# Optimization experiments

Measured on AMD Instinct MI355X. Metric: run time of the kernel, lower is better.

The kernel has to match this reference:

```python
import jax, jax.numpy as jnp
import numpy as np

N, E, FIN, C, NCLS, L = 50000, 800000, 500, 128, 7, 8
ALPHA, THETA, NEG_SLOPE = 0.1, 0.5, 0.2


def _glorot(key, shape):
    # matches torch glorot: uniform(-sqrt(6/(fan_in+fan_out)))
    std = np.sqrt(6.0 / (shape[-2] + shape[-1])).astype(np.float32)
    return jax.random.uniform(key, shape, jnp.float32, -std, std)


def setup_inputs() -> dict:
    key = jax.random.key(0)
    ks = jax.random.split(key, 12)
    x = jax.random.normal(ks[0], (N, FIN), jnp.float32)
    edge_index = jax.random.randint(ks[1], (2, E), 0, N)
    return {
        "x": x,
        "edge_index": edge_index,
        "lin0_w": _glorot(ks[2], (FIN, C)),
        "lin0_b": jnp.zeros((C,), jnp.float32),
        "lin1_w": _glorot(ks[3], (C, NCLS)),
        "lin1_b": jnp.zeros((NCLS,), jnp.float32),
        "lin_w": _glorot(ks[4], (L, C, C)),   # shared lin_l == lin_r
        "att_l": _glorot(ks[5], (L, 1, C)).reshape(L, C),
        "att_r": _glorot(ks[6], (L, 1, C)).reshape(L, C),
        "w_p": _glorot(ks[7], (L, C, C)),
        "w_n": _glorot(ks[8], (L, C, C)),
        "w1": _glorot(ks[9], (L, C, C)),
    }


def reference(x, edge_index, lin0_w, lin0_b, lin1_w, lin1_b, lin_w, att_l, att_r, w_p, w_n, w1):
    # --- gcn_norm with self loops (identical every layer since cached topology) ---
    loop = jnp.arange(N)
    src = jnp.concatenate([edge_index[0], loop])  # [E'] sources (x_j)
    dst = jnp.concatenate([edge_index[1], loop])  # [E'] targets / scatter index (x_i)
    deg = jax.ops.segment_sum(jnp.ones(src.shape[0], jnp.float32), dst, num_segments=N)
    dinv = jnp.where(deg > 0, jax.lax.rsqrt(deg), 0.0)
    ew = dinv[src] * dinv[dst]  # symmetric norm, [E']

    x0 = jax.nn.relu(x @ lin0_w + lin0_b)  # [N, C]
    betas = jnp.log(THETA / jnp.arange(1, L + 1, dtype=jnp.float32) + 1.0)

    def layer(h, params):
        lw, al, ar, wp, wn, w1l, beta = params
        xl = h @ lw                              # lin_l(x), shared for l/r
        # per-edge gate: sigmoid(leaky_relu(sigma_j + sigma_i))
        s = jax.nn.sigmoid(jax.nn.leaky_relu((xl @ al)[src] + (xl @ ar)[dst], NEG_SLOPE))
        xp = h @ wp                              # source-side features
        xn = h @ wn                              # target-side features
        msg = ew[:, None] * (xp[src] * s[:, None] + xn[dst] * (1.0 - s[:, None]))  # [E', C]
        agg = jax.ops.segment_sum(msg, dst, num_segments=N)  # scatter-add
        hn = (1.0 - ALPHA) * agg + ALPHA * x0
        out = (1.0 - beta) * hn + beta * (hn @ w1l)  # addmm with weight2=None
        return jax.nn.relu(out), s

    h, sigmas = jax.lax.scan(layer, x0, (lin_w, att_l, att_r, w_p, w_n, w1, betas))
    logits = h @ lin1_w + lin1_b
    return jax.nn.log_softmax(logits, axis=-1), sigmas
```

## Files before the change

kernel.cpp:

```cpp
#include <hip/hip_runtime.h>
#include <math.h>

constexpr int NN   = 50000;
constexpr int NE   = 800000;
constexpr int EP   = NE + NN;
constexpr int FIN  = 500;
constexpr int KPAD = 512;
constexpr int C    = 128;
constexpr int NCLS = 7;
constexpr int NL   = 8;
constexpr float ALPHA = 0.1f;
constexpr float NEG_SLOPE = 0.2f;

typedef __bf16 bf16;
typedef __bf16 bf16x8 __attribute__((ext_vector_type(8)));
typedef float  f32x4  __attribute__((ext_vector_type(4)));

__device__ inline unsigned short f2bu(float f) {
    bf16 b = (bf16)f;
    return __builtin_bit_cast(unsigned short, b);
}
__device__ inline float bulo(unsigned u) { return __builtin_bit_cast(float, u << 16); }
__device__ inline float buhi(unsigned u) { return __builtin_bit_cast(float, u & 0xffff0000u); }

__global__ void fill_i32_k(int* p, int v, int n) {
    int i = blockIdx.x * blockDim.x + threadIdx.x;
    if (i < n) p[i] = v;
}

__global__ void count_deg_k(const int* __restrict__ dst, int* __restrict__ deg, int e) {
    int i = blockIdx.x * blockDim.x + threadIdx.x;
    if (i < e) atomicAdd(&deg[dst[i]], 1);
}

__global__ void dinv_k(const int* __restrict__ deg, float* __restrict__ dinv, int n) {
    int i = blockIdx.x * blockDim.x + threadIdx.x;
    if (i < n) dinv[i] = rsqrtf((float)deg[i]);
}

constexpr int SCB = 256;
constexpr int NSB = (NN + SCB - 1) / SCB;

__global__ __launch_bounds__(SCB) void scan1_k(const int* __restrict__ deg,
                                               int* __restrict__ exoff,
                                               int* __restrict__ bsum, int n) {
    __shared__ int s[SCB];
    int t = threadIdx.x;
    int i = blockIdx.x * SCB + t;
    int v = (i < n) ? deg[i] : 0;
    s[t] = v;
    __syncthreads();
    for (int off = 1; off < SCB; off <<= 1) {
        int u = (t >= off) ? s[t - off] : 0;
        __syncthreads();
        s[t] += u;
        __syncthreads();
    }
    if (i < n) exoff[i] = s[t] - v;
    if (t == SCB - 1) bsum[blockIdx.x] = s[t];
}

__global__ __launch_bounds__(SCB) void scan2_k(const int* __restrict__ bsum,
                                               int* __restrict__ boff, int nb) {
    __shared__ int s[SCB];
    int t = threadIdx.x;
    int v = (t < nb) ? bsum[t] : 0;
    s[t] = v;
    __syncthreads();
    for (int off = 1; off < SCB; off <<= 1) {
        int u = (t >= off) ? s[t - off] : 0;
        __syncthreads();
        s[t] += u;
        __syncthreads();
    }
    if (t < nb) boff[t] = s[t] - v;
}

__global__ __launch_bounds__(SCB) void scan3_k(const int* __restrict__ exoff,
                                               const int* __restrict__ boff,
                                               int* __restrict__ offs,
                                               int* __restrict__ cursor, int n) {
    int i = blockIdx.x * SCB + threadIdx.x;
    if (i < n) {
        int o = exoff[i] + boff[blockIdx.x];
        offs[i] = o;
        cursor[i] = o;
    }
    if (i == 0) offs[n] = EP;
}

__global__ void csr_fill_k(const int* __restrict__ src, const int* __restrict__ dst,
                           const float* __restrict__ dinv, int* __restrict__ cursor,
                           int2* __restrict__ csr2, int* __restrict__ pos_of) {
    int e = blockIdx.x * blockDim.x + threadIdx.x;
    if (e >= EP) return;
    int s, d;
    if (e < NE) { s = src[e]; d = dst[e]; }
    else { s = d = e - NE; }
    float ew = dinv[s] * dinv[d];
    int pos = atomicAdd(&cursor[d], 1);
    csr2[pos] = make_int2(s, __builtin_bit_cast(int, ew));
    pos_of[e] = pos;
}

__global__ void attproj_k(const float* __restrict__ lin_w, const float* __restrict__ att_l,
                          const float* __restrict__ att_r, float* __restrict__ alp,
                          float* __restrict__ arp) {
    __shared__ float al[C], ar[C];
    int l = blockIdx.x;
    int k = threadIdx.x;
    al[k] = att_l[l * C + k];
    ar[k] = att_r[l * C + k];
    __syncthreads();
    const float* w = lin_w + (size_t)l * C * C + (size_t)k * C;
    float s1 = 0.f, s2 = 0.f;
    #pragma unroll 8
    for (int c = 0; c < C; ++c) { float v = w[c]; s1 += v * al[c]; s2 += v * ar[c]; }
    alp[l * C + k] = s1;
    arp[l * C + k] = s2;
}

__global__ void wpn_trans_k(const float* __restrict__ w_p, const float* __restrict__ w_n,
                            bf16* __restrict__ out) {
    int l = blockIdx.y;
    int nt = blockIdx.x >> 2, kb = blockIdx.x & 3;
    int lane = threadIdx.x;
    const float* W = ((nt < 8) ? w_p : w_n) + (size_t)l * C * C;
    int col = (nt & 7) * 16 + (lane & 15);
    int k0 = kb * 32 + (lane >> 4) * 8;
    bf16* o = out + (((size_t)l * 16 * 4 + (size_t)(nt * 4 + kb)) * 64 + lane) * 8;
    #pragma unroll
    for (int j = 0; j < 8; ++j) o[j] = (bf16)W[(size_t)(k0 + j) * C + col];
}

__global__ void w1_trans_k(const float* __restrict__ w1, bf16* __restrict__ out) {
    int l = blockIdx.y;
    int nt = blockIdx.x >> 2, kb = blockIdx.x & 3;
    int lane = threadIdx.x;
    const float* W = w1 + (size_t)l * C * C;
    int col = nt * 16 + (lane & 15);
    int k0 = kb * 32 + (lane >> 4) * 8;
    bf16* o = out + (((size_t)l * 8 * 4 + (size_t)(nt * 4 + kb)) * 64 + lane) * 8;
    #pragma unroll
    for (int j = 0; j < 8; ++j) o[j] = (bf16)W[(size_t)(k0 + j) * C + col];
}

__global__ void lin0_trans_k(const float* __restrict__ w, bf16* __restrict__ out) {
    int nt = blockIdx.x >> 4, kb = blockIdx.x & 15;
    int lane = threadIdx.x;
    int col = nt * 16 + (lane & 15);
    int k0 = kb * 32 + (lane >> 4) * 8;
    bf16* o = out + (((size_t)(nt * 16 + kb)) * 64 + lane) * 8;
    #pragma unroll
    for (int j = 0; j < 8; ++j) {
        int k = k0 + j;
        o[j] = (bf16)((k < FIN) ? w[(size_t)k * C + col] : 0.f);
    }
}

__global__ __launch_bounds__(256) void conv_x_k(const float* __restrict__ x,
                                                unsigned* __restrict__ xb_u) {
    int gid = blockIdx.x * blockDim.x + threadIdx.x;
    if (gid >= NN * 64) return;
    int row = gid >> 6, cg = gid & 63;
    int col = cg * 8;
    float v[8];
    if (cg < 62) {
        const float4* p = (const float4*)(x + (size_t)row * FIN + col);
        float4 a = p[0], b = p[1];
        v[0] = a.x; v[1] = a.y; v[2] = a.z; v[3] = a.w;
        v[4] = b.x; v[5] = b.y; v[6] = b.z; v[7] = b.w;
    } else {
        #pragma unroll
        for (int j = 0; j < 8; ++j)
            v[j] = (col + j < FIN) ? x[(size_t)row * FIN + col + j] : 0.f;
    }
    uint4 o;
    o.x = (unsigned)f2bu(v[0]) | ((unsigned)f2bu(v[1]) << 16);
    o.y = (unsigned)f2bu(v[2]) | ((unsigned)f2bu(v[3]) << 16);
    o.z = (unsigned)f2bu(v[4]) | ((unsigned)f2bu(v[5]) << 16);
    o.w = (unsigned)f2bu(v[6]) | ((unsigned)f2bu(v[7]) << 16);
    *(uint4*)(xb_u + (size_t)row * 256 + cg * 4) = o;
}

template <int NT, int KB, int MODE>
__global__ __launch_bounds__(256) void mgemm_k(const bf16* __restrict__ Ab,
                                               const bf16* __restrict__ Wt, int M,
                                               const float* __restrict__ bias, float beta,
                                               float* __restrict__ out_f,
                                               bf16* __restrict__ out_b,
                                               const float* __restrict__ alp,
                                               const float* __restrict__ arp,
                                               float* __restrict__ sl,
                                               float* __restrict__ sr,
                                               float* __restrict__ sig_out,
                                               const float* __restrict__ sigc,
                                               const int* __restrict__ pos_of) {
    if (MODE == 2) {
        int gid = blockIdx.x * 256 + threadIdx.x;
        int stride = gridDim.x * 256;
        for (int e = gid; e < EP; e += stride) sig_out[e] = sigc[pos_of[e]];
    }
    const int lane = threadIdx.x & 63;
    const int wv = threadIdx.x >> 6;
    const int m0 = blockIdx.x * 64 + wv * 16;
    const int mrow = lane & 15;
    const int quad = lane >> 4;
    int arow = m0 + mrow;
    if (arow >= M) arow = M - 1;
    const bf16* Arow = Ab + (size_t)arow * (KB * 32) + quad * 8;
    const bf16x8* wbase = reinterpret_cast<const bf16x8*>(Wt) + (size_t)lane;

    f32x4 acc[NT];
    #pragma unroll
    for (int t = 0; t < NT; ++t) acc[t] = (f32x4){0.f, 0.f, 0.f, 0.f};

    #pragma unroll
    for (int kb = 0; kb < KB; ++kb) {
        bf16x8 a = *reinterpret_cast<const bf16x8*>(Arow + kb * 32);
        #pragma unroll
        for (int t = 0; t < NT; ++t) {
            bf16x8 b = wbase[(size_t)(t * KB + kb) * 64];
            acc[t] = __builtin_amdgcn_mfma_f32_16x16x32_bf16(a, b, acc[t], 0, 0, 0);
        }
    }

    constexpr int NC = NT * 16;
    #pragma unroll
    for (int t = 0; t < NT; ++t) {
        int col = t * 16 + mrow;
        #pragma unroll
        for (int r = 0; r < 4; ++r) {
            int row = m0 + quad * 4 + r;
            float v = acc[t][r];
            if (MODE == 1) v = fmaxf(v + bias[col], 0.f);
            if (MODE == 2) {
                float h = (row < M) ? (float)Ab[(size_t)row * NC + col] : 0.f;
                v = fmaxf((1.f - beta) * h + beta * v, 0.f);
            }
            acc[t][r] = v;
            if (row < M) {
                if (MODE == 2 && out_f != nullptr) out_f[(size_t)row * NC + col] = v;
                out_b[(size_t)row * NC + col] = (bf16)v;
            }
        }
    }
    if ((MODE == 1 || MODE == 2) && sl != nullptr) {
        float sa[4] = {0.f, 0.f, 0.f, 0.f}, sb[4] = {0.f, 0.f, 0.f, 0.f};
        #pragma unroll
        for (int t = 0; t < NT; ++t) {
            float av = alp[t * 16 + mrow];
            float bv = arp[t * 16 + mrow];
            #pragma unroll
            for (int r = 0; r < 4; ++r) {
                sa[r] += acc[t][r] * av;
                sb[r] += acc[t][r] * bv;
            }
        }
        #pragma unroll
        for (int r = 0; r < 4; ++r) {
            #pragma unroll
            for (int m = 1; m < 16; m <<= 1) {
                sa[r] += __shfl_xor(sa[r], m);
                sb[r] += __shfl_xor(sb[r], m);
            }
        }
        if (mrow == 0) {
            #pragma unroll
            for (int r = 0; r < 4; ++r) {
                int row = m0 + quad * 4 + r;
                if (row < M) { sl[row] = sa[r]; sr[row] = sb[r]; }
            }
        }
    }
}

__global__ __launch_bounds__(256) void agg_k(const int* __restrict__ offs,
                                             const int2* __restrict__ csr2,
                                             const float* __restrict__ sl,
                                             const float* __restrict__ sr,
                                             const unsigned* __restrict__ xpnb_u,
                                             const unsigned* __restrict__ x0b_u,
                                             float* __restrict__ sigc,
                                             unsigned* __restrict__ hnb_u, int n) {
    int wid = (blockIdx.x * blockDim.x + threadIdx.x) >> 6;
    int lane = threadIdx.x & 63;
    if (wid >= n) return;
    int s0 = offs[wid], s1 = offs[wid + 1];
    float srw = sr[wid];
    const int g = lane >> 4;
    const int cg = lane & 15;
    float acc[8];
    #pragma unroll
    for (int i = 0; i < 8; ++i) acc[i] = 0.f;
    float cnl = 0.f;

    for (int j0 = s0; j0 < s1; j0 += 64) {
        int j = j0 + lane;
        int msrc = 0;
        float mcoef = 0.f;
        if (j < s1) {
            int2 e = csr2[j];
            float ew = __builtin_bit_cast(float, e.y);
            float xg = sl[e.x] + srw;
            float lr = (xg > 0.f) ? xg : NEG_SLOPE * xg;
            float sg = 1.f / (1.f + expf(-lr));
            sigc[j] = sg;
            msrc = e.x;
            mcoef = ew * sg;
            cnl += ew * (1.f - sg);
        }
        int cnt = min(64, s1 - j0);
        for (int t = 0; t < cnt; t += 4) {
            int idx = t + g;
            float coef = __shfl(mcoef, idx);
            int srcn = __shfl(msrc, idx);
            uint4 v = *(const uint4*)(xpnb_u + (size_t)srcn * 128 + cg * 4);
            acc[0] += coef * bulo(v.x);
            acc[1] += coef * buhi(v.x);
            acc[2] += coef * bulo(v.y);
            acc[3] += coef * buhi(v.y);
            acc[4] += coef * bulo(v.z);
            acc[5] += coef * buhi(v.z);
            acc[6] += coef * bulo(v.w);
            acc[7] += coef * buhi(v.w);
        }
    }
    #pragma unroll
    for (int i = 0; i < 8; ++i) {
        acc[i] += __shfl_xor(acc[i], 16);
        acc[i] += __shfl_xor(acc[i], 32);
    }
    #pragma unroll
    for (int m = 1; m < 64; m <<= 1) cnl += __shfl_xor(cnl, m);
    unsigned un = xpnb_u[(size_t)wid * 128 + 64 + cg * 4 + g];
    unsigned u0 = x0b_u[(size_t)wid * 64 + cg * 4 + g];
    float ox = (1.f - ALPHA) * (acc[g * 2] + cnl * bulo(un)) + ALPHA * bulo(u0);
    float oy = (1.f - ALPHA) * (acc[g * 2 + 1] + cnl * buhi(un)) + ALPHA * buhi(u0);
    hnb_u[(size_t)wid * 64 + cg * 4 + g] = (unsigned)f2bu(ox) | ((unsigned)f2bu(oy) << 16);
}

__global__ __launch_bounds__(256) void logits_k(const float* __restrict__ h,
                                                const float* __restrict__ w,
                                                const float* __restrict__ b,
                                                float* __restrict__ out, int n) {
    __shared__ float ws[C * NCLS];
    __shared__ float bs[NCLS];
    for (int i = threadIdx.x; i < C * NCLS; i += 256) ws[i] = w[i];
    if (threadIdx.x < NCLS) bs[threadIdx.x] = b[threadIdx.x];
    __syncthreads();
    int i = blockIdx.x * blockDim.x + threadIdx.x;
    if (i >= n) return;
    const float4* hr = (const float4*)(h + (size_t)i * C);
    float acc[NCLS];
    #pragma unroll
    for (int c = 0; c < NCLS; ++c) acc[c] = 0.f;
    for (int k4 = 0; k4 < C / 4; ++k4) {
        float4 v = hr[k4];
        int k = k4 * 4;
        #pragma unroll
        for (int c = 0; c < NCLS; ++c) {
            acc[c] += v.x * ws[k * NCLS + c] + v.y * ws[(k + 1) * NCLS + c] +
                      v.z * ws[(k + 2) * NCLS + c] + v.w * ws[(k + 3) * NCLS + c];
        }
    }
    float lg[NCLS], m = -1e30f;
    #pragma unroll
    for (int c = 0; c < NCLS; ++c) { lg[c] = acc[c] + bs[c]; m = fmaxf(m, lg[c]); }
    float sum = 0.f;
    #pragma unroll
    for (int c = 0; c < NCLS; ++c) sum += expf(lg[c] - m);
    float lse = m + logf(sum);
    #pragma unroll
    for (int c = 0; c < NCLS; ++c) out[(size_t)i * NCLS + c] = lg[c] - lse;
}

extern "C" void kernel_launch(void* const* d_in, const int* in_sizes, int n_in,
                              void* d_out, int out_size, void* d_ws, size_t ws_size,
                              hipStream_t stream) {
    (void)in_sizes; (void)n_in; (void)out_size; (void)ws_size;
    const float* x      = (const float*)d_in[0];
    const int*   eidx   = (const int*)d_in[1];
    const float* lin0_w = (const float*)d_in[2];
    const float* lin0_b = (const float*)d_in[3];
    const float* lin1_w = (const float*)d_in[4];
    const float* lin1_b = (const float*)d_in[5];
    const float* lin_w  = (const float*)d_in[6];
    const float* att_l  = (const float*)d_in[7];
    const float* att_r  = (const float*)d_in[8];
    const float* w_p    = (const float*)d_in[9];
    const float* w_n    = (const float*)d_in[10];
    const float* w1     = (const float*)d_in[11];
    float* outp = (float*)d_out;
    float* sig_base = outp + (size_t)NN * NCLS;

    const int* srcA = eidx;
    const int* dstA = eidx + NE;

    float* f = (float*)d_ws;
    float* hF   = f; f += (size_t)NN * C;
    float* sl   = f; f += NN;
    float* sr   = f; f += NN;
    float* sigc = f; f += EP;
    float* dinv = f; f += NN;
    float* alp  = f; f += NL * C;
    float* arp  = f; f += NL * C;
    f += (4 - ((NN * 2 + EP + NN + 2 * NL * C) & 3)) & 3;
    bf16* bp = (bf16*)f;
    bf16* xb    = bp;
    bf16* xpnb  = bp;  bp += (size_t)NN * 2 * C;
    bf16* hnb   = bp;  bp += (size_t)NN * C;
    bf16* hb    = bp;  bp += (size_t)NN * C;
    bf16* x0b   = bp;  bp += (size_t)NN * C;
    bf16* wpnt  = bp;  bp += (size_t)NL * 16 * 4 * 64 * 8;
    bf16* w1t   = bp;  bp += (size_t)NL * 8 * 4 * 64 * 8;
    bf16* lin0t = bp;  bp += (size_t)8 * 16 * 64 * 8;
    int* ip = (int*)bp;
    int* deg     = ip; ip += NN;
    int* offs    = ip; ip += NN + 4;
    int* cursor  = ip; ip += NN;
    int* pos_of  = ip; ip += EP;
    int* exoff   = ip; ip += NN;
    int* bsum    = ip; ip += SCB;
    int* boff    = ip; ip += SCB;
    ip += (ip - (int*)d_ws) & 1;
    int2* csr2   = (int2*)ip; ip += 2 * EP;

    dim3 B(256);
    int gN   = (NN + 255) / 256;
    int gE   = (NE + 255) / 256;
    int gEP  = (EP + 255) / 256;
    int gM64 = (NN + 63) / 64;
    int gAgg = NN / 4;

    fill_i32_k<<<gN, B, 0, stream>>>(deg, 1, NN);
    count_deg_k<<<gE, B, 0, stream>>>(dstA, deg, NE);
    dinv_k<<<gN, B, 0, stream>>>(deg, dinv, NN);
    scan1_k<<<NSB, SCB, 0, stream>>>(deg, exoff, bsum, NN);
    scan2_k<<<1, SCB, 0, stream>>>(bsum, boff, NSB);
    scan3_k<<<NSB, SCB, 0, stream>>>(exoff, boff, offs, cursor, NN);
    csr_fill_k<<<gEP, B, 0, stream>>>(srcA, dstA, dinv, cursor, csr2, pos_of);
    attproj_k<<<NL, C, 0, stream>>>(lin_w, att_l, att_r, alp, arp);

    wpn_trans_k<<<dim3(64, NL), 64, 0, stream>>>(w_p, w_n, wpnt);
    w1_trans_k<<<dim3(32, NL), 64, 0, stream>>>(w1, w1t);
    lin0_trans_k<<<128, 64, 0, stream>>>(lin0_w, lin0t);
    conv_x_k<<<(NN * 64 + 255) / 256, B, 0, stream>>>(x, (unsigned*)xb);

    mgemm_k<8, 16, 1><<<gM64, B, 0, stream>>>(xb, lin0t, NN, lin0_b, 0.f,
                                              nullptr, x0b, alp, arp, sl, sr,
                                              nullptr, nullptr, nullptr);

    const bf16* curb = x0b;
    for (int l = 0; l < NL; ++l) {
        float beta = (float)log(0.5 / (double)(l + 1) + 1.0);
        bool last = (l == NL - 1);
        mgemm_k<16, 4, 0><<<gM64, B, 0, stream>>>(curb, wpnt + (size_t)l * 16 * 4 * 64 * 8,
                                                  NN, nullptr, 0.f, nullptr, xpnb,
                                                  nullptr, nullptr, nullptr, nullptr,
                                                  nullptr, nullptr, nullptr);
        agg_k<<<gAgg, B, 0, stream>>>(offs, csr2, sl, sr, (const unsigned*)xpnb,
                                      (const unsigned*)x0b, sigc, (unsigned*)hnb, NN);
        mgemm_k<8, 4, 2><<<gM64, B, 0, stream>>>(hnb, w1t + (size_t)l * 8 * 4 * 64 * 8,
                                                 NN, nullptr, beta,
                                                 last ? hF : nullptr, hb,
                                                 last ? nullptr : (alp + (l + 1) * C),
                                                 last ? nullptr : (arp + (l + 1) * C),
                                                 last ? nullptr : sl,
                                                 last ? nullptr : sr,
                                                 sig_base + (size_t)l * EP, sigc, pos_of);
        curb = hb;
    }

    logits_k<<<gN, B, 0, stream>>>(hF, lin1_w, lin1_b, outp, NN);
}
```

Measured before the change: 981.0 us.

## Recompute per-edge sigmoid in original order instead of caching via pos_of scatter

Removes the sigc cache and pos_of permutation. Sigmas are now recomputed directly in original edge order inside the MODE 0 GEMM prologue from sl/sr and the raw edge index, so agg_k no longer writes per-edge sigmoid values. Setup kernels are also consolidated: the degree fill and dinv kernels are folded into a memset and scan1, and the three weight-transpose kernels become one pack kernel. A zero-coefficient skip is added in the gather loop. The trade-off is duplicated sigmoid math and random sl/sr reads in exchange for less memory traffic and fewer launches.

Result: slower. 1.218 ms (+24.1%).

```diff
diff --git a/kernel.cpp b/kernel.cpp
--- a/kernel.cpp
+++ b/kernel.cpp
@@ -5,7 +5,6 @@
 constexpr int NE   = 800000;
 constexpr int EP   = NE + NN;
 constexpr int FIN  = 500;
-constexpr int KPAD = 512;
 constexpr int C    = 128;
 constexpr int NCLS = 7;
 constexpr int NL   = 8;
@@ -23,31 +22,23 @@
 __device__ inline float bulo(unsigned u) { return __builtin_bit_cast(float, u << 16); }
 __device__ inline float buhi(unsigned u) { return __builtin_bit_cast(float, u & 0xffff0000u); }
 
-__global__ void fill_i32_k(int* p, int v, int n) {
-    int i = blockIdx.x * blockDim.x + threadIdx.x;
-    if (i < n) p[i] = v;
-}
-
 __global__ void count_deg_k(const int* __restrict__ dst, int* __restrict__ deg, int e) {
     int i = blockIdx.x * blockDim.x + threadIdx.x;
     if (i < e) atomicAdd(&deg[dst[i]], 1);
 }
 
-__global__ void dinv_k(const int* __restrict__ deg, float* __restrict__ dinv, int n) {
-    int i = blockIdx.x * blockDim.x + threadIdx.x;
-    if (i < n) dinv[i] = rsqrtf((float)deg[i]);
-}
-
 constexpr int SCB = 256;
 constexpr int NSB = (NN + SCB - 1) / SCB;
 
 __global__ __launch_bounds__(SCB) void scan1_k(const int* __restrict__ deg,
                                                int* __restrict__ exoff,
-                                               int* __restrict__ bsum, int n) {
+                                               int* __restrict__ bsum,
+                                               float* __restrict__ dinv, int n) {
     __shared__ int s[SCB];
     int t = threadIdx.x;
     int i = blockIdx.x * SCB + t;
-    int v = (i < n) ? deg[i] : 0;
+    int v = (i < n) ? deg[i] + 1 : 0;
+    if (i < n) dinv[i] = rsqrtf((float)v);
     s[t] = v;
     __syncthreads();
     for (int off = 1; off < SCB; off <<= 1) {
@@ -91,7 +82,7 @@
 
 __global__ void csr_fill_k(const int* __restrict__ src, const int* __restrict__ dst,
                            const float* __restrict__ dinv, int* __restrict__ cursor,
-                           int2* __restrict__ csr2, int* __restrict__ pos_of) {
+                           int2* __restrict__ csr2) {
     int e = blockIdx.x * blockDim.x + threadIdx.x;
     if (e >= EP) return;
     int s, d;
@@ -100,7 +91,6 @@
     float ew = dinv[s] * dinv[d];
     int pos = atomicAdd(&cursor[d], 1);
     csr2[pos] = make_int2(s, __builtin_bit_cast(int, ew));
-    pos_of[e] = pos;
 }
 
 __global__ void attproj_k(const float* __restrict__ lin_w, const float* __restrict__ att_l,
@@ -120,41 +110,42 @@
     arp[l * C + k] = s2;
 }
 
-__global__ void wpn_trans_k(const float* __restrict__ w_p, const float* __restrict__ w_n,
-                            bf16* __restrict__ out) {
-    int l = blockIdx.y;
-    int nt = blockIdx.x >> 2, kb = blockIdx.x & 3;
+__global__ void pack_k(const float* __restrict__ w_p, const float* __restrict__ w_n,
+                       const float* __restrict__ w1, const float* __restrict__ lin0_w,
+                       bf16* __restrict__ wpnt, bf16* __restrict__ w1t,
+                       bf16* __restrict__ lin0t) {
+    int b = blockIdx.x;
     int lane = threadIdx.x;
-    const float* W = ((nt < 8) ? w_p : w_n) + (size_t)l * C * C;
-    int col = (nt & 7) * 16 + (lane & 15);
-    int k0 = kb * 32 + (lane >> 4) * 8;
-    bf16* o = out + (((size_t)l * 16 * 4 + (size_t)(nt * 4 + kb)) * 64 + lane) * 8;
-    #pragma unroll
-    for (int j = 0; j < 8; ++j) o[j] = (bf16)W[(size_t)(k0 + j) * C + col];
-}
-
-__global__ void w1_trans_k(const float* __restrict__ w1, bf16* __restrict__ out) {
-    int l = blockIdx.y;
-    int nt = blockIdx.x >> 2, kb = blockIdx.x & 3;
-    int lane = threadIdx.x;
-    const float* W = w1 + (size_t)l * C * C;
-    int col = nt * 16 + (lane & 15);
-    int k0 = kb * 32 + (lane >> 4) * 8;
-    bf16* o = out + (((size_t)l * 8 * 4 + (size_t)(nt * 4 + kb)) * 64 + lane) * 8;
-    #pragma unroll
-    for (int j = 0; j < 8; ++j) o[j] = (bf16)W[(size_t)(k0 + j) * C + col];
-}
-
-__global__ void lin0_trans_k(const float* __restrict__ w, bf16* __restrict__ out) {
-    int nt = blockIdx.x >> 4, kb = blockIdx.x & 15;
-    int lane = threadIdx.x;
-    int col = nt * 16 + (lane & 15);
-    int k0 = kb * 32 + (lane >> 4) * 8;
-    bf16* o = out + (((size_t)(nt * 16 + kb)) * 64 + lane) * 8;
-    #pragma unroll
-    for (int j = 0; j < 8; ++j) {
-        int k = k0 + j;
-        o[j] = (bf16)((k < FIN) ? w[(size_t)k * C + col] : 0.f);
+    if (b < NL * 64) {
+        int l = b >> 6, inner = b & 63;
+        int nt = inner >> 2, kb = inner & 3;
+        const float* W = ((nt < 8) ? w_p : w_n) + (size_t)l * C * C;
+        int col = (nt & 7) * 16 + (lane & 15);
+        int k0 = kb * 32 + (lane >> 4) * 8;
+        bf16* o = wpnt + (((size_t)l * 64 + inner) * 64 + lane) * 8;
+        #pragma unroll
+        for (int j = 0; j < 8; ++j) o[j] = (bf16)W[(size_t)(k0 + j) * C + col];
+    } else if (b < NL * 96) {
+        int idx = b - NL * 64;
+        int l = idx >> 5, inner = idx & 31;
+        int nt = inner >> 2, kb = inner & 3;
+        const float* W = w1 + (size_t)l * C * C;
+        int col = nt * 16 + (lane & 15);
+        int k0 = kb * 32 + (lane >> 4) * 8;
+        bf16* o = w1t + (((size_t)l * 32 + inner) * 64 + lane) * 8;
+        #pragma unroll
+        for (int j = 0; j < 8; ++j) o[j] = (bf16)W[(size_t)(k0 + j) * C + col];
+    } else {
+        int idx = b - NL * 96;
+        int nt = idx >> 4, kb = idx & 15;
+        int col = nt * 16 + (lane & 15);
+        int k0 = kb * 32 + (lane >> 4) * 8;
+        bf16* o = lin0t + (((size_t)(nt * 16 + kb)) * 64 + lane) * 8;
+        #pragma unroll
+        for (int j = 0; j < 8; ++j) {
+            int k = k0 + j;
+            o[j] = (bf16)((k < FIN) ? lin0_w[(size_t)k * C + col] : 0.f);
+        }
     }
 }
 
@@ -194,12 +185,19 @@
                                                float* __restrict__ sl,
                                                float* __restrict__ sr,
                                                float* __restrict__ sig_out,
-                                               const float* __restrict__ sigc,
-                                               const int* __restrict__ pos_of) {
-    if (MODE == 2) {
+                                               const int* __restrict__ srcA,
+                                               const int* __restrict__ dstA) {
+    if (MODE == 0) {
         int gid = blockIdx.x * 256 + threadIdx.x;
         int stride = gridDim.x * 256;
-        for (int e = gid; e < EP; e += stride) sig_out[e] = sigc[pos_of[e]];
+        for (int e = gid; e < EP; e += stride) {
+            int s, d;
+            if (e < NE) { s = srcA[e]; d = dstA[e]; }
+            else { s = d = e - NE; }
+            float xg = sl[s] + sr[d];
+            float lr = (xg > 0.f) ? xg : NEG_SLOPE * xg;
+            sig_out[e] = 1.f / (1.f + expf(-lr));
+        }
     }
     const int lane = threadIdx.x & 63;
     const int wv = threadIdx.x >> 6;
@@ -245,7 +243,7 @@
             }
         }
     }
-    if ((MODE == 1 || MODE == 2) && sl != nullptr) {
+    if ((MODE == 1 || MODE == 2) && alp != nullptr) {
         float sa[4] = {0.f, 0.f, 0.f, 0.f}, sb[4] = {0.f, 0.f, 0.f, 0.f};
         #pragma unroll
         for (int t = 0; t < NT; ++t) {
@@ -281,7 +279,6 @@
                                              const float* __restrict__ sr,
                                              const unsigned* __restrict__ xpnb_u,
                                              const unsigned* __restrict__ x0b_u,
-                                             float* __restrict__ sigc,
                                              unsigned* __restrict__ hnb_u, int n) {
     int wid = (blockIdx.x * blockDim.x + threadIdx.x) >> 6;
     int lane = threadIdx.x & 63;
@@ -305,7 +302,6 @@
             float xg = sl[e.x] + srw;
             float lr = (xg > 0.f) ? xg : NEG_SLOPE * xg;
             float sg = 1.f / (1.f + expf(-lr));
-            sigc[j] = sg;
             msrc = e.x;
             mcoef = ew * sg;
             cnl += ew * (1.f - sg);
@@ -315,15 +311,17 @@
             int idx = t + g;
             float coef = __shfl(mcoef, idx);
             int srcn = __shfl(msrc, idx);
-            uint4 v = *(const uint4*)(xpnb_u + (size_t)srcn * 128 + cg * 4);
-            acc[0] += coef * bulo(v.x);
-            acc[1] += coef * buhi(v.x);
-            acc[2] += coef * bulo(v.y);
-            acc[3] += coef * buhi(v.y);
-            acc[4] += coef * bulo(v.z);
-            acc[5] += coef * buhi(v.z);
-            acc[6] += coef * bulo(v.w);
-            acc[7] += coef * buhi(v.w);
+            if (coef != 0.f) {
+                uint4 v = *(const uint4*)(xpnb_u + (size_t)srcn * 128 + cg * 4);
+                acc[0] += coef * bulo(v.x);
+                acc[1] += coef * buhi(v.x);
+                acc[2] += coef * bulo(v.y);
+                acc[3] += coef * buhi(v.y);
+                acc[4] += coef * bulo(v.z);
+                acc[5] += coef * buhi(v.z);
+                acc[6] += coef * bulo(v.w);
+                acc[7] += coef * buhi(v.w);
+            }
         }
     }
     #pragma unroll
@@ -401,11 +399,10 @@
     float* hF   = f; f += (size_t)NN * C;
     float* sl   = f; f += NN;
     float* sr   = f; f += NN;
-    float* sigc = f; f += EP;
     float* dinv = f; f += NN;
     float* alp  = f; f += NL * C;
     float* arp  = f; f += NL * C;
-    f += (4 - ((NN * 2 + EP + NN + 2 * NL * C) & 3)) & 3;
+    f = (float*)(((uintptr_t)f + 15) & ~(uintptr_t)15);
     bf16* bp = (bf16*)f;
     bf16* xb    = bp;
     bf16* xpnb  = bp;  bp += (size_t)NN * 2 * C;
@@ -419,12 +416,11 @@
     int* deg     = ip; ip += NN;
     int* offs    = ip; ip += NN + 4;
     int* cursor  = ip; ip += NN;
-    int* pos_of  = ip; ip += EP;
     int* exoff   = ip; ip += NN;
     int* bsum    = ip; ip += SCB;
     int* boff    = ip; ip += SCB;
-    ip += (ip - (int*)d_ws) & 1;
-    int2* csr2   = (int2*)ip; ip += 2 * EP;
+    ip = (int*)(((uintptr_t)ip + 7) & ~(uintptr_t)7);
+    int2* csr2   = (int2*)ip;
 
     dim3 B(256);
     int gN   = (NN + 255) / 256;
@@ -433,18 +429,15 @@
     int gM64 = (NN + 63) / 64;
     int gAgg = NN / 4;
 
-    fill_i32_k<<<gN, B, 0, stream>>>(deg, 1, NN);
+    hipMemsetAsync(deg, 0, (size_t)NN * sizeof(int), stream);
     count_deg_k<<<gE, B, 0, stream>>>(dstA, deg, NE);
-    dinv_k<<<gN, B, 0, stream>>>(deg, dinv, NN);
-    scan1_k<<<NSB, SCB, 0, stream>>>(deg, exoff, bsum, NN);
+    scan1_k<<<NSB, SCB, 0, stream>>>(deg, exoff, bsum, dinv, NN);
     scan2_k<<<1, SCB, 0, stream>>>(bsum, boff, NSB);
     scan3_k<<<NSB, SCB, 0, stream>>>(exoff, boff, offs, cursor, NN);
-    csr_fill_k<<<gEP, B, 0, stream>>>(srcA, dstA, dinv, cursor, csr2, pos_of);
+    csr_fill_k<<<gEP, B, 0, stream>>>(srcA, dstA, dinv, cursor, csr2);
     attproj_k<<<NL, C, 0, stream>>>(lin_w, att_l, att_r, alp, arp);
 
-    wpn_trans_k<<<dim3(64, NL), 64, 0, stream>>>(w_p, w_n, wpnt);
-    w1_trans_k<<<dim3(32, NL), 64, 0, stream>>>(w1, w1t);
-    lin0_trans_k<<<128, 64, 0, stream>>>(lin0_w, lin0t);
+    pack_k<<<NL * 96 + 128, 64, 0, stream>>>(w_p, w_n, w1, lin0_w, wpnt, w1t, lin0t);
     conv_x_k<<<(NN * 64 + 255) / 256, B, 0, stream>>>(x, (unsigned*)xb);
 
     mgemm_k<8, 16, 1><<<gM64, B, 0, stream>>>(xb, lin0t, NN, lin0_b, 0.f,
@@ -457,10 +450,10 @@
         bool last = (l == NL - 1);
         mgemm_k<16, 4, 0><<<gM64, B, 0, stream>>>(curb, wpnt + (size_t)l * 16 * 4 * 64 * 8,
                                                   NN, nullptr, 0.f, nullptr, xpnb,
-                                                  nullptr, nullptr, nullptr, nullptr,
-                                                  nullptr, nullptr, nullptr);
+                                                  nullptr, nullptr, sl, sr,
+                                                  sig_base + (size_t)l * EP, srcA, dstA);
         agg_k<<<gAgg, B, 0, stream>>>(offs, csr2, sl, sr, (const unsigned*)xpnb,
-                                      (const unsigned*)x0b, sigc, (unsigned*)hnb, NN);
+                                      (const unsigned*)x0b, (unsigned*)hnb, NN);
         mgemm_k<8, 4, 2><<<gM64, B, 0, stream>>>(hnb, w1t + (size_t)l * 8 * 4 * 64 * 8,
                                                  NN, nullptr, beta,
                                                  last ? hF : nullptr, hb,
@@ -468,7 +461,7 @@
                                                  last ? nullptr : (arp + (l + 1) * C),
                                                  last ? nullptr : sl,
                                                  last ? nullptr : sr,
-                                                 sig_base + (size_t)l * EP, sigc, pos_of);
+                                                 nullptr, nullptr, nullptr);
         curb = hb;
     }
 
```
